# Performance work log

Measured on AMD Instinct MI355X. Metric: run time of the kernel, lower is better.

The kernel has to match this reference:

```python
import jax, jax.numpy as jnp
import numpy as np

# ---- config (matches init_kwargs) ----
SPATIAL_SCALE = 0.0625
POOLED = 7
OUT_DIM = 256
SAMPLE_PER_PART = 4
TRANS_STD = 0.1
PART_SIZE = 7
DEFORM_FC_DIM = 1024
# group_size == 1 -> position-sensitive group index is always 0, channel c == ctop


def _deform_roi_pool(feat, rois, offset, no_trans):
    """Faithful JAX port of DeformablePSROIPoolForward (DCNv2), group_size=1.
    feat: (B,C,H,W), rois: (N,5)=[b,x1,y1,x2,y2], offset: (N,2,P,P) or None.
    Returns (N,C,P,P)."""
    B, C, H, W = feat.shape
    N = rois.shape[0]
    P, S = POOLED, SAMPLE_PER_PART
    dt = feat.dtype
    featT = jnp.transpose(feat, (0, 2, 3, 1))  # (B,H,W,C) for spatial gathers

    b = rois[:, 0].astype(jnp.int32)
    rsw = jnp.round(rois[:, 1]) * SPATIAL_SCALE - 0.5
    rsh = jnp.round(rois[:, 2]) * SPATIAL_SCALE - 0.5
    rew = (jnp.round(rois[:, 3]) + 1.0) * SPATIAL_SCALE - 0.5
    reh = (jnp.round(rois[:, 4]) + 1.0) * SPATIAL_SCALE - 0.5
    roi_w = jnp.maximum(rew - rsw, 0.1)
    roi_h = jnp.maximum(reh - rsh, 0.1)
    bin_h = roi_h / P            # (N,)
    bin_w = roi_w / P
    sub_h = bin_h / S
    sub_w = bin_w / S

    ph = jnp.arange(P)
    pw = jnp.arange(P)
    part_h = jnp.floor(ph.astype(dt) / P * PART_SIZE).astype(jnp.int32)  # == ph when part_size==P
    part_w = jnp.floor(pw.astype(dt) / P * PART_SIZE).astype(jnp.int32)

    if no_trans:
        tx = jnp.zeros((N, P, P), dt)
        ty = jnp.zeros((N, P, P), dt)
    else:
        tx = offset[:, 0][:, part_h][:, :, part_w] * TRANS_STD  # (N,P,P)
        ty = offset[:, 1][:, part_h][:, :, part_w] * TRANS_STD

    hstart = ph.astype(dt)[None, :, None] * bin_h[:, None, None] + rsh[:, None, None] + ty * roi_h[:, None, None]
    wstart = pw.astype(dt)[None, None, :] * bin_w[:, None, None] + rsw[:, None, None] + tx * roi_w[:, None, None]

    ih = jnp.arange(S).astype(dt)
    iw = jnp.arange(S).astype(dt)
    # sample coords, shape (N,P,P,S,S); ih along axis -2, iw along axis -1
    h = hstart[..., None, None] + ih[:, None] * sub_h[:, None, None, None, None]
    w = wstart[..., None, None] + iw[None, :] * sub_w[:, None, None, None, None]

    valid = (w >= -0.5) & (w <= W - 0.5) & (h >= -0.5) & (h <= H - 0.5)
    hc = jnp.clip(h, 0.0, H - 1.0)
    wc = jnp.clip(w, 0.0, W - 1.0)
    h0 = jnp.floor(hc).astype(jnp.int32)
    w0 = jnp.floor(wc).astype(jnp.int32)
    h1 = jnp.minimum(h0 + 1, H - 1)
    w1 = jnp.minimum(w0 + 1, W - 1)
    lh = hc - h0.astype(dt)
    lw = wc - w0.astype(dt)

    bidx = b[:, None, None, None, None]

    def g(yy, xx):  # (N,P,P,S,S,C)
        return featT[bidx, yy, xx]

    val = (g(h0, w0) * ((1 - lh) * (1 - lw))[..., None]
           + g(h0, w1) * ((1 - lh) * lw)[..., None]
           + g(h1, w0) * (lh * (1 - lw))[..., None]
           + g(h1, w1) * (lh * lw)[..., None])
    val = jnp.where(valid[..., None], val, jnp.zeros((), dt))
    ssum = val.sum(axis=(3, 4))                       # (N,P,P,C)
    cnt = valid.sum(axis=(3, 4)).astype(dt)           # (N,P,P)
    out = jnp.where(cnt[..., None] > 0, ssum / jnp.maximum(cnt, 1.0)[..., None], jnp.zeros((), dt))
    return jnp.transpose(out, (0, 3, 1, 2))           # (N,C,P,P)


def setup_inputs() -> dict:
    key = jax.random.key(0)
    ks = jax.random.split(key, 12)
    B, C, H, W = 2, OUT_DIM, 100, 100
    N = 512
    img = H / SPATIAL_SCALE  # 1600

    feat = jax.random.normal(ks[0], (B, C, H, W), jnp.float32)

    bi = jax.random.randint(ks[1], (N,), 0, B).astype(jnp.float32)
    x1 = jax.random.uniform(ks[2], (N,), jnp.float32, 0.0, img - 420.0)
    y1 = jax.random.uniform(ks[3], (N,), jnp.float32, 0.0, img - 420.0)
    x2 = x1 + jax.random.uniform(ks[4], (N,), jnp.float32, 32.0, 400.0)
    y2 = y1 + jax.random.uniform(ks[5], (N,), jnp.float32, 32.0, 400.0)
    rois = jnp.stack([bi, x1, y1, x2, y2], axis=1)

    fin = POOLED * POOLED * OUT_DIM  # 12544
    w1 = jax.random.normal(ks[6], (DEFORM_FC_DIM, fin), jnp.float32) / np.sqrt(fin)
    b1 = jnp.zeros((DEFORM_FC_DIM,), jnp.float32)
    w2 = jax.random.normal(ks[7], (DEFORM_FC_DIM, DEFORM_FC_DIM), jnp.float32) / np.sqrt(DEFORM_FC_DIM)
    b2 = jnp.zeros((DEFORM_FC_DIM,), jnp.float32)
    # original init zeroes the last layer; use small random so offsets/mask are non-trivial
    w3 = jax.random.normal(ks[8], (POOLED * POOLED * 3, DEFORM_FC_DIM), jnp.float32) * 0.01
    b3 = jnp.zeros((POOLED * POOLED * 3,), jnp.float32)
    return {"input": feat, "rois": rois, "w1": w1, "b1": b1, "w2": w2, "b2": b2, "w3": w3, "b3": b3}


def reference(input, rois, w1, b1, w2, b2, w3, b3):
    N = rois.shape[0]
    P = POOLED
    # pass 1: plain (no_trans) deformable RoI pooling to predict offsets/mask
    roi0 = _deform_roi_pool(input, rois, None, no_trans=True)      # (N,C,P,P)
    x = roi0.reshape(N, -1)
    x = jax.nn.relu(x @ w1.T + b1)
    x = jax.nn.relu(x @ w2.T + b2)
    om = (x @ w3.T + b3).reshape(N, 3, P, P)
    offset = om[:, 0:2]                                            # (N,2,P,P) [trans_x, trans_y]
    mask = jax.nn.sigmoid(om[:, 2:3])                              # (N,1,P,P)
    # pass 2: deformable pooling with learned offsets, modulated by mask
    out = _deform_roi_pool(input, rois, offset, no_trans=False) * mask
    return out
```

## Files before the change

### kernel.cpp

```cpp
#include <hip/hip_runtime.h>

#define BB 2
#define CC 256
#define HH 100
#define WW 100
#define NROI 512
#define KDIM 12544
#define FC 1024

typedef _Float16 half_t;
typedef _Float16 f16x2 __attribute__((ext_vector_type(2)));
typedef _Float16 f16x8 __attribute__((ext_vector_type(8)));
typedef _Float16 f16x4 __attribute__((ext_vector_type(4)));
typedef float f32x4 __attribute__((ext_vector_type(4)));

__device__ __forceinline__ void gload16(const half_t* g, half_t* l) {
  __builtin_amdgcn_global_load_lds(
      (const __attribute__((address_space(1))) unsigned int*)g,
      (__attribute__((address_space(3))) unsigned int*)l, 16, 0, 0);
}

__global__ __launch_bounds__(256) void transpose_feat(const float* __restrict__ feat,
                                                      half_t* __restrict__ featT) {
  __shared__ float tile[32][33];
  int b = blockIdx.z;
  int hw0 = blockIdx.x * 32;
  int c0 = blockIdx.y * 32;
  int tx = threadIdx.x, ty = threadIdx.y;
  const float* fb = feat + (size_t)b * CC * (HH * WW);
#pragma unroll
  for (int i = 0; i < 4; i++) {
    int c = c0 + ty + i * 8;
    int hw = hw0 + tx;
    tile[ty + i * 8][tx] = (hw < HH * WW) ? fb[(size_t)c * (HH * WW) + hw] : 0.0f;
  }
  __syncthreads();
  half_t* ob = featT + (size_t)b * (HH * WW) * CC;
#pragma unroll
  for (int i = 0; i < 4; i++) {
    int hw = hw0 + ty + i * 8;
    int c = c0 + tx;
    if (hw < HH * WW) ob[(size_t)hw * CC + c] = (half_t)tile[tx][ty + i * 8];
  }
}

__global__ __launch_bounds__(256) void convert_f32_f16(const float* __restrict__ in,
                                                       half_t* __restrict__ out, int n) {
  int i4 = (blockIdx.x * 256 + threadIdx.x) * 4;
  if (i4 < n) {
    float4 v = *(const float4*)(in + i4);
    f16x4 o;
    o[0] = (half_t)v.x; o[1] = (half_t)v.y; o[2] = (half_t)v.z; o[3] = (half_t)v.w;
    *(f16x4*)(out + i4) = o;
  }
}

struct PixW { int idx; float w; };

template <bool PASS2>
__global__ __launch_bounds__(512) void pool_kernel(const half_t* __restrict__ featT,
                                                   const float* __restrict__ rois,
                                                   const float* __restrict__ om,
                                                   half_t* __restrict__ xout,
                                                   float* __restrict__ out) {
  __shared__ PixW s_pix[49 * 28];
  __shared__ int s_cnt[49];
  __shared__ float s_scale[49];
  __shared__ float  s_outf[PASS2 ? KDIM : 1];
  __shared__ half_t s_outh[PASS2 ? 1 : KDIM];

  const int n = blockIdx.x;
  const int tid = threadIdx.x;
  const float* r = rois + n * 5;
  const int b = (int)r[0];
  const float rsw = rintf(r[1]) * 0.0625f - 0.5f;
  const float rsh = rintf(r[2]) * 0.0625f - 0.5f;
  const float rew = (rintf(r[3]) + 1.0f) * 0.0625f - 0.5f;
  const float reh = (rintf(r[4]) + 1.0f) * 0.0625f - 0.5f;
  const float roi_w = fmaxf(rew - rsw, 0.1f);
  const float roi_h = fmaxf(reh - rsh, 0.1f);
  const float bin_h = roi_h / 7.0f, bin_w = roi_w / 7.0f;
  const float sub_h = bin_h * 0.25f, sub_w = bin_w * 0.25f;
  const half_t* fb = featT + (size_t)b * (HH * WW) * CC;

  if (tid < 49) {
    const int p = tid, ph = p / 7, pw = p - ph * 7;
    float tx = 0.0f, ty = 0.0f, mask = 1.0f;
    if (PASS2) {
      tx = om[n * 147 + p] * 0.1f;
      ty = om[n * 147 + 49 + p] * 0.1f;
      mask = 1.0f / (1.0f + expf(-om[n * 147 + 98 + p]));
    }
    const float hst = (float)ph * bin_h + rsh + ty * roi_h;
    const float wst = (float)pw * bin_w + rsw + tx * roi_w;
    float wh[6] = {0, 0, 0, 0, 0, 0};
    float hc0 = fminf(fmaxf(hst, 0.0f), 99.0f);
    const int r0 = (int)hc0;
    int rtop = r0;
    float vsh = 0.0f;
#pragma unroll
    for (int i = 0; i < 4; i++) {
      float h = hst + (float)i * sub_h;
      bool v = (h >= -0.5f) && (h <= (float)HH - 0.5f);
      float hc = fminf(fmaxf(h, 0.0f), 99.0f);
      int h0 = (int)hc;
      float lh = hc - (float)h0;
      int h1 = min(h0 + 1, HH - 1);
      if (v) { wh[h0 - r0] += 1.0f - lh; wh[h1 - r0] += lh; vsh += 1.0f; }
      rtop = h1;
    }
    float wwc[6] = {0, 0, 0, 0, 0, 0};
    float wc0 = fminf(fmaxf(wst, 0.0f), 99.0f);
    const int c0 = (int)wc0;
    int ctop = c0;
    float vsw = 0.0f;
#pragma unroll
    for (int j = 0; j < 4; j++) {
      float w = wst + (float)j * sub_w;
      bool v = (w >= -0.5f) && (w <= (float)WW - 0.5f);
      float wc = fminf(fmaxf(w, 0.0f), 99.0f);
      int w0 = (int)wc;
      float lw = wc - (float)w0;
      int w1 = min(w0 + 1, WW - 1);
      if (v) { wwc[w0 - c0] += 1.0f - lw; wwc[w1 - c0] += lw; vsw += 1.0f; }
      ctop = w1;
    }
    const int nr = rtop - r0 + 1, nc = ctop - c0 + 1;
    float cntf = vsh * vsw;
    s_scale[p] = (cntf > 0.0f) ? mask / cntf : 0.0f;
    PixW* dst = &s_pix[p * 28];
    int m = 0;
    for (int ri = 0; ri < nr; ri++) {
      int rowoff = (r0 + ri) * WW + c0;
      for (int ci = 0; ci < nc; ci++) {
        dst[m].idx = (rowoff + ci) * CC;
        dst[m].w = wh[ri] * wwc[ci];
        m++;
      }
    }
    while (m & 3) { dst[m].idx = 0; dst[m].w = 0.0f; m++; }
    s_cnt[p] = m;
  }
  __syncthreads();

  const int wv = tid >> 6;
  const int c4 = (tid & 63) * 4;
  for (int p = wv; p < 49; p += 8) {
    const int cnt = __builtin_amdgcn_readfirstlane(s_cnt[p]);
    const PixW* cp = &s_pix[p * 28];
    float a0 = 0.0f, a1 = 0.0f, a2 = 0.0f, a3 = 0.0f;
    for (int q = 0; q < cnt; q += 4) {
#pragma unroll
      for (int u = 0; u < 4; u++) {
        PixW e = cp[q + u];
        int si = __builtin_amdgcn_readfirstlane(e.idx);
        float sw = __uint_as_float(__builtin_amdgcn_readfirstlane(__float_as_uint(e.w)));
        f16x4 v = *(const f16x4*)(fb + si + c4);
        a0 += sw * (float)v[0];
        a1 += sw * (float)v[1];
        a2 += sw * (float)v[2];
        a3 += sw * (float)v[3];
      }
    }
    float sc = s_scale[p];
    a0 *= sc; a1 *= sc; a2 *= sc; a3 *= sc;
    if (PASS2) {
      s_outf[(c4 + 0) * 49 + p] = a0;
      s_outf[(c4 + 1) * 49 + p] = a1;
      s_outf[(c4 + 2) * 49 + p] = a2;
      s_outf[(c4 + 3) * 49 + p] = a3;
    } else {
      s_outh[(c4 + 0) * 49 + p] = (half_t)a0;
      s_outh[(c4 + 1) * 49 + p] = (half_t)a1;
      s_outh[(c4 + 2) * 49 + p] = (half_t)a2;
      s_outh[(c4 + 3) * 49 + p] = (half_t)a3;
    }
  }
  __syncthreads();

  if (PASS2) {
    float* ob = out + (size_t)n * KDIM;
    for (int l = tid * 4; l < KDIM; l += 2048)
      *(float4*)(ob + l) = *(const float4*)(s_outf + l);
  } else {
    half_t* ob = xout + (size_t)n * KDIM;
    for (int l = tid * 8; l < KDIM; l += 4096)
      *(f16x8*)(ob + l) = *(const f16x8*)(s_outh + l);
  }
}

template <int SK>
__global__ __launch_bounds__(256, 2) void gemm_lds(const half_t* __restrict__ A,
                                                   const half_t* __restrict__ B,
                                                   float* __restrict__ P, int K) {
  __shared__ half_t As[2][128 * 64];
  __shared__ half_t Bs[2][128 * 64];
  const int d = blockIdx.x + gridDim.x * (blockIdx.y + gridDim.y * blockIdx.z);
  const int g = (d & 7) * (SK * 4) + (d >> 3);
  const int z = g >> 5;
  const int tile = g & 31;
  const int m0 = (tile & 3) * 128;
  const int n0 = (tile >> 2) * 128;
  const int Kc = K / SK;
  const int kbeg = z * Kc;
  const int tid = threadIdx.x;
  const int lane = tid & 63;
  const int wave = tid >> 6;
  const int wm = (wave & 1) * 64;
  const int wn = (wave >> 1) * 64;
  const int fr = lane & 15;
  const int kc0 = lane >> 4;
  const int lr = lane >> 3;
  const int lc = (lane & 7) ^ lr;
  const half_t* Ag = A + (size_t)(m0 + wave * 8 + lr) * K + kbeg + lc * 8;
  const half_t* Bg = B + (size_t)(n0 + wave * 8 + lr) * K + kbeg + lc * 8;
  f32x4 acc[4][4] = {};

  auto stage = [&](int buf, int ko) {
#pragma unroll
    for (int s = 0; s < 4; s++)
      gload16(Ag + (size_t)(32 * s) * K + ko, &As[buf][s * 2048 + wave * 512]);
#pragma unroll
    for (int s = 0; s < 4; s++)
      gload16(Bg + (size_t)(32 * s) * K + ko, &Bs[buf][s * 2048 + wave * 512]);
  };

  const int iters = Kc >> 6;
  stage(0, 0);
  if (iters > 1) {
    stage(1, 64);
    asm volatile("s_waitcnt vmcnt(8)" ::: "memory");
  } else {
    asm volatile("s_waitcnt vmcnt(0)" ::: "memory");
  }
  __builtin_amdgcn_s_barrier();

  for (int it = 0; it < iters; it++) {
    const int cur = it & 1;
#pragma unroll
    for (int ks = 0; ks < 2; ks++) {
      const int swz = ((kc0 + ks * 4) ^ (fr & 7)) * 8;
      f16x8 af[4], bf[4];
#pragma unroll
      for (int i = 0; i < 4; i++) af[i] = *(const f16x8*)&As[cur][(wm + i * 16 + fr) * 64 + swz];
#pragma unroll
      for (int j = 0; j < 4; j++) bf[j] = *(const f16x8*)&Bs[cur][(wn + j * 16 + fr) * 64 + swz];
#pragma unroll
      for (int i = 0; i < 4; i++)
#pragma unroll
        for (int j = 0; j < 4; j++)
          acc[i][j] = __builtin_amdgcn_mfma_f32_16x16x32_f16(af[i], bf[j], acc[i][j], 0, 0, 0);
    }
    asm volatile("s_waitcnt lgkmcnt(0)" ::: "memory");
    __builtin_amdgcn_s_barrier();
    const bool issue = (it + 2 < iters);
    if (issue) stage(cur, (it + 2) * 64);
    if (it + 1 < iters) {
      if (issue) asm volatile("s_waitcnt vmcnt(8)" ::: "memory");
      else       asm volatile("s_waitcnt vmcnt(0)" ::: "memory");
      __builtin_amdgcn_s_barrier();
    }
  }
  float* Pz = P + (((size_t)z * 32 + tile) * 4 + wave) * 4096;
#pragma unroll
  for (int i = 0; i < 4; i++)
#pragma unroll
    for (int j = 0; j < 4; j++)
#pragma unroll
      for (int rr = 0; rr < 4; rr++)
        Pz[((i * 4 + j) * 4 + rr) * 64 + lane] = acc[i][j][rr];
}

template <bool OUT16, bool RELU, int SK>
__global__ __launch_bounds__(256) void reduce_blocked(const float* __restrict__ P,
                                                      const float* __restrict__ bias,
                                                      void* __restrict__ out,
                                                      int MN, int N) {
  int i4 = (blockIdx.x * 256 + threadIdx.x) * 4;
  if (i4 >= MN) return;
  float4 s = *(const float4*)(P + i4);
#pragma unroll
  for (int z = 1; z < SK; z++) {
    float4 t = *(const float4*)(P + (size_t)z * MN + i4);
    s.x += t.x; s.y += t.y; s.z += t.z; s.w += t.w;
  }
  const int lane0 = i4 & 63;
  const int q     = (i4 >> 6) & 63;
  const int wave  = (i4 >> 12) & 3;
  const int bx    = (i4 >> 14) & 3;
  const int by    = (i4 >> 16) & 7;
  const int rr = q & 3, j_ = (q >> 2) & 3, i_ = q >> 4;
  const int row = bx * 128 + (wave & 1) * 64 + i_ * 16 + (lane0 >> 4) * 4 + rr;
  const int col = by * 128 + (wave >> 1) * 64 + j_ * 16 + (lane0 & 15);
  float4 bv = *(const float4*)(bias + col);
  s.x += bv.x; s.y += bv.y; s.z += bv.z; s.w += bv.w;
  if (RELU) {
    s.x = fmaxf(s.x, 0.0f); s.y = fmaxf(s.y, 0.0f);
    s.z = fmaxf(s.z, 0.0f); s.w = fmaxf(s.w, 0.0f);
  }
  size_t o = (size_t)row * N + col;
  if (OUT16) {
    f16x4 ov;
    ov[0] = (half_t)s.x; ov[1] = (half_t)s.y; ov[2] = (half_t)s.z; ov[3] = (half_t)s.w;
    *(f16x4*)((half_t*)out + o) = ov;
  } else {
    *(float4*)((float*)out + o) = s;
  }
}

__global__ __launch_bounds__(192) void gemm_small(const float* __restrict__ h2,
                                                  const float* __restrict__ w3,
                                                  const float* __restrict__ b3,
                                                  float* __restrict__ om) {
  __shared__ float hs[FC];
  int n = blockIdx.x;
  for (int k = threadIdx.x; k < FC; k += 192) hs[k] = h2[(size_t)n * FC + k];
  __syncthreads();
  int j = threadIdx.x;
  if (j < 147) {
    float acc = b3[j];
    const float* wr = w3 + (size_t)j * FC;
    for (int k = 0; k < FC; k += 4) {
      float4 wv = *(const float4*)(wr + k);
      acc += hs[k] * wv.x + hs[k + 1] * wv.y + hs[k + 2] * wv.z + hs[k + 3] * wv.w;
    }
    om[n * 147 + j] = acc;
  }
}

extern "C" void kernel_launch(void* const* d_in, const int* in_sizes, int n_in,
                              void* d_out, int out_size, void* d_ws, size_t ws_size,
                              hipStream_t stream) {
  const float* feat = (const float*)d_in[0];
  const float* rois = (const float*)d_in[1];
  const float* w1 = (const float*)d_in[2];
  const float* b1 = (const float*)d_in[3];
  const float* w2 = (const float*)d_in[4];
  const float* b2 = (const float*)d_in[5];
  const float* w3 = (const float*)d_in[6];
  const float* b3 = (const float*)d_in[7];
  float* out = (float*)d_out;
  char* ws = (char*)d_ws;

  half_t* featT = (half_t*)ws;
  half_t* xh    = (half_t*)(ws + 10240000);
  half_t* w1h   = (half_t*)(ws + 23085056);
  half_t* w2h   = (half_t*)(ws + 48775168);
  half_t* h1    = (half_t*)(ws + 50872320);
  float*  h2    = (float*)(ws + 51920896);
  float*  omb   = (float*)(ws + 54018048);
  float*  part  = (float*)(ws + 54319104);

  const int MN = NROI * FC;

  transpose_feat<<<dim3(313, 8, 2), dim3(32, 8), 0, stream>>>(feat, featT);
  convert_f32_f16<<<dim3(12544), dim3(256), 0, stream>>>(w1, w1h, FC * KDIM);
  convert_f32_f16<<<dim3(1024), dim3(256), 0, stream>>>(w2, w2h, FC * FC);
  pool_kernel<false><<<dim3(NROI), dim3(512), 0, stream>>>(featT, rois, nullptr, xh, nullptr);

  gemm_lds<14><<<dim3(4, 8, 14), dim3(256), 0, stream>>>(xh, w1h, part, KDIM);
  reduce_blocked<true, true, 14><<<dim3(MN / 1024), dim3(256), 0, stream>>>(part, b1, (void*)h1, MN, FC);

  gemm_lds<8><<<dim3(4, 8, 8), dim3(256), 0, stream>>>(h1, w2h, part, FC);
  reduce_blocked<false, true, 8><<<dim3(MN / 1024), dim3(256), 0, stream>>>(part, b2, (void*)h2, MN, FC);

  gemm_small<<<dim3(NROI), dim3(192), 0, stream>>>(h2, w3, b3, omb);
  pool_kernel<true><<<dim3(NROI), dim3(512), 0, stream>>>(featT, rois, omb, nullptr, out);
}
```

Baseline: 255.4 us.

## Split third FC layer over K and batch rows, fuse reduction into pool pass

The small third GEMM now computes 8 RoIs per block and splits K into 8 chunks of 128, writing partial sums. This reuses each w3 row across 8 RoIs and spreads the work over more blocks. The partial-sum reduction and bias add move into the second pooling kernel's setup threads, which saves one intermediate write and read. The cost is 8 scattered partial loads per bin in the pool kernel.

```diff
diff --git a/kernel.cpp b/kernel.cpp
--- a/kernel.cpp
+++ b/kernel.cpp
@@ -60,7 +60,8 @@
 template <bool PASS2>
 __global__ __launch_bounds__(512) void pool_kernel(const half_t* __restrict__ featT,
                                                    const float* __restrict__ rois,
-                                                   const float* __restrict__ om,
+                                                   const float* __restrict__ part3,
+                                                   const float* __restrict__ b3,
                                                    half_t* __restrict__ xout,
                                                    float* __restrict__ out) {
   __shared__ PixW s_pix[49 * 28];
@@ -87,9 +88,15 @@
     const int p = tid, ph = p / 7, pw = p - ph * 7;
     float tx = 0.0f, ty = 0.0f, mask = 1.0f;
     if (PASS2) {
-      tx = om[n * 147 + p] * 0.1f;
-      ty = om[n * 147 + 49 + p] * 0.1f;
-      mask = 1.0f / (1.0f + expf(-om[n * 147 + 98 + p]));
+      float o0 = b3[p], o1 = b3[49 + p], o2 = b3[98 + p];
+#pragma unroll
+      for (int zz = 0; zz < 8; zz++) {
+        const float* pz = part3 + ((size_t)zz * NROI + n) * 147;
+        o0 += pz[p]; o1 += pz[49 + p]; o2 += pz[98 + p];
+      }
+      tx = o0 * 0.1f;
+      ty = o1 * 0.1f;
+      mask = 1.0f / (1.0f + expf(-o2));
     }
     const float hst = (float)ph * bin_h + rsh + ty * roi_h;
     const float wst = (float)pw * bin_w + rsw + tx * roi_w;
@@ -308,23 +315,32 @@
   }
 }
 
-__global__ __launch_bounds__(192) void gemm_small(const float* __restrict__ h2,
+__global__ __launch_bounds__(192) void gemm3_part(const float* __restrict__ h2,
                                                   const float* __restrict__ w3,
-                                                  const float* __restrict__ b3,
-                                                  float* __restrict__ om) {
-  __shared__ float hs[FC];
-  int n = blockIdx.x;
-  for (int k = threadIdx.x; k < FC; k += 192) hs[k] = h2[(size_t)n * FC + k];
+                                                  float* __restrict__ part3) {
+  __shared__ float hs[8][128];
+  const int n0 = blockIdx.x * 8;
+  const int z = blockIdx.y;
+  const int tid = threadIdx.x;
+  for (int idx = tid; idx < 1024; idx += 192) {
+    int nn = idx >> 7, kk = idx & 127;
+    hs[nn][kk] = h2[(size_t)(n0 + nn) * FC + z * 128 + kk];
+  }
   __syncthreads();
-  int j = threadIdx.x;
+  const int j = tid;
   if (j < 147) {
-    float acc = b3[j];
-    const float* wr = w3 + (size_t)j * FC;
-    for (int k = 0; k < FC; k += 4) {
+    const float* wr = w3 + (size_t)j * FC + z * 128;
+    float acc[8] = {0, 0, 0, 0, 0, 0, 0, 0};
+    for (int k = 0; k < 128; k += 4) {
       float4 wv = *(const float4*)(wr + k);
-      acc += hs[k] * wv.x + hs[k + 1] * wv.y + hs[k + 2] * wv.z + hs[k + 3] * wv.w;
-    }
-    om[n * 147 + j] = acc;
+#pragma unroll
+      for (int nn = 0; nn < 8; nn++)
+        acc[nn] += hs[nn][k] * wv.x + hs[nn][k + 1] * wv.y +
+                   hs[nn][k + 2] * wv.z + hs[nn][k + 3] * wv.w;
+    }
+#pragma unroll
+    for (int nn = 0; nn < 8; nn++)
+      part3[((size_t)z * NROI + n0 + nn) * 147 + j] = acc[nn];
   }
 }
 
@@ -348,7 +364,6 @@
   half_t* w2h   = (half_t*)(ws + 48775168);
   half_t* h1    = (half_t*)(ws + 50872320);
   float*  h2    = (float*)(ws + 51920896);
-  float*  omb   = (float*)(ws + 54018048);
   float*  part  = (float*)(ws + 54319104);
 
   const int MN = NROI * FC;
@@ -356,7 +371,7 @@
   transpose_feat<<<dim3(313, 8, 2), dim3(32, 8), 0, stream>>>(feat, featT);
   convert_f32_f16<<<dim3(12544), dim3(256), 0, stream>>>(w1, w1h, FC * KDIM);
   convert_f32_f16<<<dim3(1024), dim3(256), 0, stream>>>(w2, w2h, FC * FC);
-  pool_kernel<false><<<dim3(NROI), dim3(512), 0, stream>>>(featT, rois, nullptr, xh, nullptr);
+  pool_kernel<false><<<dim3(NROI), dim3(512), 0, stream>>>(featT, rois, nullptr, nullptr, xh, nullptr);
 
   gemm_lds<14><<<dim3(4, 8, 14), dim3(256), 0, stream>>>(xh, w1h, part, KDIM);
   reduce_blocked<true, true, 14><<<dim3(MN / 1024), dim3(256), 0, stream>>>(part, b1, (void*)h1, MN, FC);
@@ -364,6 +379,6 @@
   gemm_lds<8><<<dim3(4, 8, 8), dim3(256), 0, stream>>>(h1, w2h, part, FC);
   reduce_blocked<false, true, 8><<<dim3(MN / 1024), dim3(256), 0, stream>>>(part, b2, (void*)h2, MN, FC);
 
-  gemm_small<<<dim3(NROI), dim3(192), 0, stream>>>(h2, w3, b3, omb);
-  pool_kernel<true><<<dim3(NROI), dim3(512), 0, stream>>>(featT, rois, omb, nullptr, out);
-}
+  gemm3_part<<<dim3(64, 8), dim3(192), 0, stream>>>(h2, w3, part);
+  pool_kernel<true><<<dim3(NROI), dim3(512), 0, stream>>>(featT, rois, part, b3, nullptr, out);
+}
```

Result: faster. 229.4 us (-10.2%).
